# Kernel tuning notes

Measured on AMD Instinct MI355X. Metric: run time of the kernel, lower is better.

Reference implementation:

```python
import jax, jax.numpy as jnp
import numpy as np

LATENT = 256
MID = 512
T = 5          # num_transforms
OUT = T * 6 + T  # 35
THRESH = 0.9   # MATRIX_NORM_THRESHOLD
EPS = 1e-5     # torch LayerNorm eps
B = 131072


def _xavier(key, fan_in, fan_out):
    lim = np.sqrt(6.0 / (fan_in + fan_out)).astype(np.float32)
    return jax.random.uniform(key, (fan_in, fan_out), jnp.float32, -lim, lim)


def setup_inputs() -> dict:
    key = jax.random.key(0)
    ks = jax.random.split(key, 8)
    z = jax.random.normal(ks[0], (B, LATENT), jnp.float32)
    W1 = _xavier(ks[1], LATENT, MID)
    Wa = _xavier(ks[2], MID, MID)
    Wb = _xavier(ks[3], MID, MID)
    Wout = _xavier(ks[4], MID, OUT)
    bias = lambda n: jnp.full((n,), 0.01, jnp.float32)  # nn.init.constant_(bias, 0.01)
    return {
        "z": z,
        "W1": W1, "b1": bias(MID), "g1": jnp.ones((MID,), jnp.float32), "be1": jnp.zeros((MID,), jnp.float32),
        "Wa": Wa, "ba": bias(MID), "ga": jnp.ones((MID,), jnp.float32), "bea": jnp.zeros((MID,), jnp.float32),
        "Wb": Wb, "bb": bias(MID), "gb": jnp.ones((MID,), jnp.float32), "beb": jnp.zeros((MID,), jnp.float32),
        "Wout": Wout, "bout": bias(OUT),
    }


def _layernorm(x, g, b):
    mu = jnp.mean(x, axis=-1, keepdims=True)
    var = jnp.mean(jnp.square(x - mu), axis=-1, keepdims=True)
    return (x - mu) * jax.lax.rsqrt(var + EPS) * g + b


def reference(z, W1, b1, g1, be1, Wa, ba, ga, bea, Wb, bb, gb, beb, Wout, bout):
    # Linear -> LayerNorm -> ReLU
    h = jax.nn.relu(_layernorm(z @ W1 + b1, g1, be1))
    # ResidualBlock: Linear -> LN -> SiLU -> Linear -> LN, then skip add
    y = jax.nn.silu(_layernorm(h @ Wa + ba, ga, bea))
    y = _layernorm(y @ Wb + bb, gb, beb)
    h = h + y
    x = h @ Wout + bout                     # [B, 35]

    affines = x[:, : T * 6].reshape(-1, T, 2, 3)  # [B, T, 2, 3]
    logits = x[:, T * 6:]                         # [B, T]
    probs = jax.nn.softmax(logits, axis=-1)

    M = affines[..., :2]                          # [B, T, 2, 2]
    U, S, Vh = jnp.linalg.svd(M, full_matrices=False)
    Sc = jnp.minimum(S, THRESH)                   # clamp(max=0.9)
    M2 = jnp.einsum("btij,btj,btjk->btik", U, Sc, Vh)
    affines = jnp.concatenate([M2, affines[..., 2:]], axis=-1)
    return affines, probs
```

## Files before the change

### kernel.cpp

```cpp
#include <hip/hip_runtime.h>
#include <hip/hip_bf16.h>

#define BQ     131072
#define NT     5

typedef unsigned short u16;
typedef unsigned int   u32;
typedef unsigned long long u64;
typedef __attribute__((ext_vector_type(8))) short bf16x8;
typedef __attribute__((ext_vector_type(4))) float f32x4;
typedef __attribute__((ext_vector_type(2))) float f32x2;

__device__ __forceinline__ u16 f2bf(float x) {
  union { float f; u32 u; } v; v.f = x;
  u32 r = (v.u + 0x7FFFu + ((v.u >> 16) & 1u)) >> 16;
  return (u16)r;
}

__global__ __launch_bounds__(256) void transpose_cast(
    const float* __restrict__ src, u16* __restrict__ dst, int K, int N, int NP) {
  __shared__ float tile[32][33];
  int kx = blockIdx.x * 32, ny = blockIdx.y * 32;
  int tx = threadIdx.x, ty = threadIdx.y;
#pragma unroll
  for (int i = 0; i < 4; i++) {
    int k = kx + ty + i * 8, n = ny + tx;
    tile[ty + i * 8][tx] = (k < K && n < N) ? src[(size_t)k * N + n] : 0.f;
  }
  __syncthreads();
#pragma unroll
  for (int i = 0; i < 4; i++) {
    int n = ny + ty + i * 8, k = kx + tx;
    if (n < NP && k < K) dst[(size_t)n * K + k] = f2bf(tile[tx][ty + i * 8]);
  }
}

template <int K, int ACT>
__device__ __forceinline__ void layer(
    const u16* __restrict__ wt, const float* __restrict__ bias,
    const float* __restrict__ gam, const float* __restrict__ bet,
    const u16* src, u16* dst, float* sStat,
    int lane, int wid, int l15, int lg, int wfb)
{
  f32x4 acc[2][4];
#pragma unroll
  for (int m = 0; m < 2; m++)
#pragma unroll
    for (int n = 0; n < 4; n++) acc[m][n] = (f32x4){0.f, 0.f, 0.f, 0.f};

#pragma unroll
  for (int kb = 0; kb < K; kb += 32) {
    const int k0 = kb + lg * 8;
    bf16x8 a[2];
#pragma unroll
    for (int m = 0; m < 2; m++)
      a[m] = *(const bf16x8*)(wt + (size_t)(wfb + m * 16 + l15) * K + k0);
    bf16x8 bv[4];
#pragma unroll
    for (int n = 0; n < 4; n++) {
      int b = n * 16 + l15;
      int byte = (b * (K * 2) + k0 * 2) ^ ((b & 7) << 4);
      bv[n] = *(const bf16x8*)((const char*)src + byte);
    }
    __builtin_amdgcn_s_setprio(1);
#pragma unroll
    for (int m = 0; m < 2; m++)
#pragma unroll
      for (int n = 0; n < 4; n++)
        acc[m][n] = __builtin_amdgcn_mfma_f32_16x16x32_bf16(a[m], bv[n], acc[m][n], 0, 0, 0);
    __builtin_amdgcn_s_setprio(0);
  }

#pragma unroll
  for (int m = 0; m < 2; m++) {
    f32x4 bv4 = *(const f32x4*)(bias + wfb + m * 16 + lg * 4);
#pragma unroll
    for (int n = 0; n < 4; n++)
#pragma unroll
      for (int r = 0; r < 4; r++) acc[m][n][r] += bv4[r];
  }

  float s[4], q[4];
#pragma unroll
  for (int n = 0; n < 4; n++) {
    s[n] = 0.f; q[n] = 0.f;
#pragma unroll
    for (int m = 0; m < 2; m++)
#pragma unroll
      for (int r = 0; r < 4; r++) { float v = acc[m][n][r]; s[n] += v; q[n] += v * v; }
    s[n] += __shfl_xor(s[n], 16); q[n] += __shfl_xor(q[n], 16);
    s[n] += __shfl_xor(s[n], 32); q[n] += __shfl_xor(q[n], 32);
  }
  if (lg == 0) {
#pragma unroll
    for (int n = 0; n < 4; n++) {
      int b = n * 16 + l15;
      *(f32x2*)(sStat + wid * 128 + b * 2) = (f32x2){s[n], q[n]};
    }
  }
  __syncthreads();

  float ss = 0.f, qq = 0.f;
#pragma unroll
  for (int w = 0; w < 16; w++) {
    f32x2 v = *(const f32x2*)(sStat + w * 128 + lane * 2);
    ss += v[0]; qq += v[1];
  }
  float meanb = ss * (1.f / 512.f);
  float rstdb = rsqrtf(qq * (1.f / 512.f) - meanb * meanb + 1e-5f);

  float mean[4], rstd[4];
#pragma unroll
  for (int n = 0; n < 4; n++) {
    mean[n] = __shfl(meanb, n * 16 + l15);
    rstd[n] = __shfl(rstdb, n * 16 + l15);
  }

#pragma unroll
  for (int m = 0; m < 2; m++) {
    int f0 = wfb + m * 16 + lg * 4;
    f32x4 gv  = *(const f32x4*)(gam + f0);
    f32x4 bev = *(const f32x4*)(bet + f0);
#pragma unroll
    for (int n = 0; n < 4; n++) {
      int b = n * 16 + l15;
      u16 pk[4];
#pragma unroll
      for (int r = 0; r < 4; r++) {
        float v = (acc[m][n][r] - mean[n]) * rstd[n] * gv[r] + bev[r];
        if (ACT == 1) v = fmaxf(v, 0.f);
        else if (ACT == 2) v = v / (1.f + __expf(-v));
        pk[r] = f2bf(v);
      }
      u64 w64 = (u64)pk[0] | ((u64)pk[1] << 16) | ((u64)pk[2] << 32) | ((u64)pk[3] << 48);
      int byte = (b * 1024 + f0 * 2) ^ ((b & 7) << 4);
      *(u64*)((char*)dst + byte) = w64;
    }
  }
  __syncthreads();
}

__global__ __launch_bounds__(1024)
__attribute__((amdgpu_waves_per_eu(4))) void ifs_main(
    const float* __restrict__ z,
    const u16* __restrict__ wt1, const u16* __restrict__ wta,
    const u16* __restrict__ wtb, const u16* __restrict__ wtout,
    const float* __restrict__ b1, const float* __restrict__ g1, const float* __restrict__ be1,
    const float* __restrict__ ba, const float* __restrict__ ga, const float* __restrict__ bea,
    const float* __restrict__ bb, const float* __restrict__ gb, const float* __restrict__ beb,
    const float* __restrict__ bout, float* __restrict__ out)
{
  __shared__ __align__(16) char smem[65536 * 2 + 8192];
  u16*   sA    = (u16*)smem;
  u16*   sB    = (u16*)(smem + 65536);
  float* sStat = (float*)(smem + 131072);

  const int tid  = threadIdx.x;
  const int lane = tid & 63, wid = tid >> 6;
  const int l15  = lane & 15, lg = lane >> 4;
  const int bbase = blockIdx.x * 64;
  const int wfb   = wid * 32;

#pragma unroll
  for (int i = 0; i < 4; i++) {
    int c = tid + i * 1024;
    int b = c >> 6, kc = c & 63;
    const float4 v = *(const float4*)(z + (size_t)(bbase + b) * 256 + kc * 4);
    u32 lo = (u32)f2bf(v.x) | ((u32)f2bf(v.y) << 16);
    u32 hi = (u32)f2bf(v.z) | ((u32)f2bf(v.w) << 16);
    u64 pk = (u64)lo | ((u64)hi << 32);
    int byte = (b * 512 + kc * 8) ^ ((b & 7) << 4);
    *(u64*)((char*)sB + byte) = pk;
  }
  __syncthreads();

  layer<256, 1>(wt1, b1, g1, be1, sB, sA, sStat, lane, wid, l15, lg, wfb);
  layer<512, 2>(wta, ba, ga, bea, sA, sB, sStat, lane, wid, l15, lg, wfb);
  layer<512, 0>(wtb, bb, gb, beb, sB, sB, sStat, lane, wid, l15, lg, wfb);

  {
    const int nf = wid & 3, kh = wid >> 2;
    const int b  = nf * 16 + l15;
    f32x4 xacc[3];
#pragma unroll
    for (int m = 0; m < 3; m++) xacc[m] = (f32x4){0.f, 0.f, 0.f, 0.f};
#pragma unroll
    for (int kk = 0; kk < 128; kk += 32) {
      int k0 = kh * 128 + kk + lg * 8;
      int byte = (b * 1024 + k0 * 2) ^ ((b & 7) << 4);
      bf16x8 bh = *(const bf16x8*)((const char*)sA + byte);
      bf16x8 by = *(const bf16x8*)((const char*)sB + byte);
#pragma unroll
      for (int m = 0; m < 3; m++) {
        bf16x8 aw = *(const bf16x8*)(wtout + (size_t)(m * 16 + l15) * 512 + k0);
        xacc[m] = __builtin_amdgcn_mfma_f32_16x16x32_bf16(aw, bh, xacc[m], 0, 0, 0);
        xacc[m] = __builtin_amdgcn_mfma_f32_16x16x32_bf16(aw, by, xacc[m], 0, 0, 0);
      }
    }
    __syncthreads();
    float* sP = (float*)sA;
#pragma unroll
    for (int m = 0; m < 3; m++)
      *(f32x4*)(sP + (size_t)(kh * 64 + b) * 48 + m * 16 + lg * 4) = xacc[m];
    __syncthreads();
    float* sX = (float*)sB;
    if (tid < 768) {
      int b2 = tid / 12, j = (tid - b2 * 12) * 4;
      f32x4 v0 = *(const f32x4*)(sP + (size_t)(0 * 64 + b2) * 48 + j);
      f32x4 v1 = *(const f32x4*)(sP + (size_t)(1 * 64 + b2) * 48 + j);
      f32x4 v2 = *(const f32x4*)(sP + (size_t)(2 * 64 + b2) * 48 + j);
      f32x4 v3 = *(const f32x4*)(sP + (size_t)(3 * 64 + b2) * 48 + j);
#pragma unroll
      for (int r = 0; r < 4; r++) v0[r] += v1[r] + v2[r] + v3[r];
      *(f32x4*)(sX + (size_t)b2 * 48 + j) = v0;
    }
    __syncthreads();

    if (tid < 64) {
      int bb2 = tid;
      float l[5], mx = -1e30f;
#pragma unroll
      for (int j = 0; j < 5; j++) { l[j] = sX[bb2 * 48 + 30 + j] + bout[30 + j]; mx = fmaxf(mx, l[j]); }
      float ssum = 0.f, e[5];
#pragma unroll
      for (int j = 0; j < 5; j++) { e[j] = __expf(l[j] - mx); ssum += e[j]; }
      float inv = 1.f / ssum;
      float* op = out + (size_t)BQ * 30 + (size_t)(bbase + bb2) * 5;
#pragma unroll
      for (int j = 0; j < 5; j++) op[j] = e[j] * inv;
    }
    if (tid < 320) {
      int b2 = tid / 5, t = tid - b2 * 5;
      const float* xr = sX + b2 * 48 + t * 6;
      float a   = xr[0] + bout[t * 6 + 0];
      float bb_ = xr[1] + bout[t * 6 + 1];
      float tx  = xr[2] + bout[t * 6 + 2];
      float c   = xr[3] + bout[t * 6 + 3];
      float d   = xr[4] + bout[t * 6 + 4];
      float ty  = xr[5] + bout[t * 6 + 5];
      float E = 0.5f * (a + d), F = 0.5f * (a - d);
      float G = 0.5f * (c + bb_), H = 0.5f * (c - bb_);
      float Q = sqrtf(E * E + H * H), R = sqrtf(F * F + G * G);
      float sx = Q + R, sy = Q - R;
      float a1 = atan2f(G, F), a2 = atan2f(H, E);
      float th = 0.5f * (a2 - a1), ph = 0.5f * (a2 + a1);
      float sxc = fminf(sx, 0.9f);
      float syc = fminf(fmaxf(sy, -0.9f), 0.9f);
      float st, ct, sp, cp;
      __sincosf(th, &st, &ct);
      __sincosf(ph, &sp, &cp);
      float ux = cp * sxc, uy = sp * sxc, vx = sp * syc, vy = cp * syc;
      float m00 =  ux * ct - vx * st;
      float m01 = -ux * st - vx * ct;
      float m10 =  uy * ct + vy * st;
      float m11 = -uy * st + vy * ct;
      float* op = out + (size_t)(bbase + b2) * 30 + t * 6;
      op[0] = m00; op[1] = m01; op[2] = tx;
      op[3] = m10; op[4] = m11; op[5] = ty;
    }
  }
}

extern "C" void kernel_launch(void* const* d_in, const int* in_sizes, int n_in,
                              void* d_out, int out_size, void* d_ws, size_t ws_size,
                              hipStream_t stream) {
  const float* z    = (const float*)d_in[0];
  const float* W1   = (const float*)d_in[1];
  const float* b1   = (const float*)d_in[2];
  const float* g1   = (const float*)d_in[3];
  const float* be1  = (const float*)d_in[4];
  const float* Wa   = (const float*)d_in[5];
  const float* ba   = (const float*)d_in[6];
  const float* ga   = (const float*)d_in[7];
  const float* bea  = (const float*)d_in[8];
  const float* Wb   = (const float*)d_in[9];
  const float* bb   = (const float*)d_in[10];
  const float* gb   = (const float*)d_in[11];
  const float* beb  = (const float*)d_in[12];
  const float* Wout = (const float*)d_in[13];
  const float* bout = (const float*)d_in[14];
  float* out = (float*)d_out;

  char* w = (char*)d_ws;
  u16* wt1   = (u16*)(w);
  u16* wta   = (u16*)(w + 262144);
  u16* wtb   = (u16*)(w + 786432);
  u16* wtout = (u16*)(w + 1310720);

  dim3 tb(32, 8);
  transpose_cast<<<dim3(8, 16),  tb, 0, stream>>>(W1,   wt1,   256, 512, 512);
  transpose_cast<<<dim3(16, 16), tb, 0, stream>>>(Wa,   wta,   512, 512, 512);
  transpose_cast<<<dim3(16, 16), tb, 0, stream>>>(Wb,   wtb,   512, 512, 512);
  transpose_cast<<<dim3(16, 2),  tb, 0, stream>>>(Wout, wtout, 512, 35,  48);

  ifs_main<<<BQ / 64, 1024, 0, stream>>>(
      z, wt1, wta, wtb, wtout,
      b1, g1, be1, ba, ga, bea, bb, gb, beb, bout, out);
}
```

Baseline: 686.7 us.

## Stage weight K-slabs into LDS via double-buffered global_load_lds and split head pass

Each layer now streams its weights through LDS. Weights are pre-laid-out in swizzled 32-wide K slabs and copied with double-buffered global_load_lds, instead of each wave loading its weights from global memory directly. Activations are kept in a single in-place buffer. To allow this, the output head is split into two passes: one on h right after layer 1, and one on y that adds the saved partial result. The four weight prep kernels are merged into one launch. The changes add a barrier and vmcnt wait per K step, and the larger LDS footprint limits occupancy to one block per CU.

```diff
diff --git a/kernel.cpp b/kernel.cpp
--- a/kernel.cpp
+++ b/kernel.cpp
@@ -1,8 +1,8 @@
 #include <hip/hip_runtime.h>
 #include <hip/hip_bf16.h>
 
-#define BQ     131072
-#define NT     5
+#define BQ 131072
+#define NT 5
 
 typedef unsigned short u16;
 typedef unsigned int   u32;
@@ -11,64 +11,120 @@
 typedef __attribute__((ext_vector_type(4))) float f32x4;
 typedef __attribute__((ext_vector_type(2))) float f32x2;
 
+#define ACT_OFF   0
+#define WBUF_OFF  65536
+#define SX_OFF    (WBUF_OFF + 53248)
+#define XH_OFF    131072
+#define STAT_OFF  143360
+#define SMEM_SZ   151552
+
 __device__ __forceinline__ u16 f2bf(float x) {
   union { float f; u32 u; } v; v.f = x;
   u32 r = (v.u + 0x7FFFu + ((v.u >> 16) & 1u)) >> 16;
   return (u16)r;
 }
 
-__global__ __launch_bounds__(256) void transpose_cast(
-    const float* __restrict__ src, u16* __restrict__ dst, int K, int N, int NP) {
-  __shared__ float tile[32][33];
+__device__ __forceinline__ int wsw(int f, int k) {
+  return (f * 64 + k * 2) ^ ((f & 7) << 4);
+}
+
+__global__ __launch_bounds__(256) void prep_weights(
+    const float* __restrict__ s0, const float* __restrict__ s1,
+    const float* __restrict__ s2, const float* __restrict__ s3,
+    u16* __restrict__ d0, u16* __restrict__ d1,
+    u16* __restrict__ d2, u16* __restrict__ d3) {
+  const int zid = blockIdx.z;
   int kx = blockIdx.x * 32, ny = blockIdx.y * 32;
   int tx = threadIdx.x, ty = threadIdx.y;
-#pragma unroll
-  for (int i = 0; i < 4; i++) {
-    int k = kx + ty + i * 8, n = ny + tx;
-    tile[ty + i * 8][tx] = (k < K && n < N) ? src[(size_t)k * N + n] : 0.f;
-  }
-  __syncthreads();
-#pragma unroll
-  for (int i = 0; i < 4; i++) {
-    int n = ny + ty + i * 8, k = kx + tx;
-    if (n < NP && k < K) dst[(size_t)n * K + k] = f2bf(tile[tx][ty + i * 8]);
+  if (zid < 3) {
+    const float* src = (zid == 0) ? s0 : ((zid == 1) ? s1 : s2);
+    u16* dst         = (zid == 0) ? d0 : ((zid == 1) ? d1 : d2);
+    const int K = (zid == 0) ? 256 : 512;
+    if (kx >= K) return;
+#pragma unroll
+    for (int i = 0; i < 4; i++) {
+      int k = kx + ty + i * 8, n = ny + tx;
+      if (k < K) {
+        u16 v = f2bf(src[(size_t)k * 512 + n]);
+        size_t byte = (size_t)(k >> 5) * 32768 + (u32)wsw(n, k & 31);
+        *(u16*)((char*)dst + byte) = v;
+      }
+    }
+  } else {
+    if (ny >= 48) return;
+    __shared__ float tile[32][33];
+#pragma unroll
+    for (int i = 0; i < 4; i++) {
+      int k = kx + ty + i * 8, n = ny + tx;
+      tile[ty + i * 8][tx] = (k < 512 && n < 35) ? s3[(size_t)k * 35 + n] : 0.f;
+    }
+    __syncthreads();
+#pragma unroll
+    for (int i = 0; i < 4; i++) {
+      int n = ny + ty + i * 8, k = kx + tx;
+      if (n < 48) d3[(size_t)n * 512 + k] = f2bf(tile[tx][ty + i * 8]);
+    }
+  }
+}
+
+__device__ __forceinline__ void stage_slab(const u16* __restrict__ wsrc,
+                                           char* ldsdst, int wid, int lane) {
+#pragma unroll
+  for (int i = 0; i < 2; i++) {
+    int off = (wid * 2 + i) * 1024;
+    __builtin_amdgcn_global_load_lds(
+        (const __attribute__((address_space(1))) void*)((const char*)wsrc + off + lane * 16),
+        (__attribute__((address_space(3))) void*)(ldsdst + off), 16, 0, 0);
   }
 }
 
 template <int K, int ACT>
 __device__ __forceinline__ void layer(
-    const u16* __restrict__ wt, const float* __restrict__ bias,
+    const u16* __restrict__ wslabs, const float* __restrict__ bias,
     const float* __restrict__ gam, const float* __restrict__ bet,
-    const u16* src, u16* dst, float* sStat,
-    int lane, int wid, int l15, int lg, int wfb)
+    const char* src, char* dst, char* smem,
+    int tid, int lane, int wid, int l15, int lg, int wfb)
 {
+  char* wbuf   = smem + WBUF_OFF;
+  float* sStat = (float*)(smem + STAT_OFF);
+  const int SS = (K == 256) ? 512 : 1024;
+
   f32x4 acc[2][4];
 #pragma unroll
   for (int m = 0; m < 2; m++)
 #pragma unroll
     for (int n = 0; n < 4; n++) acc[m][n] = (f32x4){0.f, 0.f, 0.f, 0.f};
 
-#pragma unroll
-  for (int kb = 0; kb < K; kb += 32) {
-    const int k0 = kb + lg * 8;
-    bf16x8 a[2];
-#pragma unroll
-    for (int m = 0; m < 2; m++)
-      a[m] = *(const bf16x8*)(wt + (size_t)(wfb + m * 16 + l15) * K + k0);
+  stage_slab(wslabs, wbuf, wid, lane);
+  asm volatile("s_waitcnt vmcnt(0)" ::: "memory");
+  __syncthreads();
+
+  const int aoff0 = wsw(wfb + l15, lg * 8);
+  const int aoff1 = wsw(wfb + 16 + l15, lg * 8);
+  const int NS = K / 32;
+  for (int t = 0; t < NS; ++t) {
+    const char* slab = wbuf + (t & 1) * 32768;
+    if (t + 1 < NS)
+      stage_slab(wslabs + (size_t)(t + 1) * 16384, wbuf + ((t + 1) & 1) * 32768, wid, lane);
+    const int k0 = t * 32 + lg * 8;
+    bf16x8 a0 = *(const bf16x8*)(slab + aoff0);
+    bf16x8 a1 = *(const bf16x8*)(slab + aoff1);
     bf16x8 bv[4];
 #pragma unroll
     for (int n = 0; n < 4; n++) {
       int b = n * 16 + l15;
-      int byte = (b * (K * 2) + k0 * 2) ^ ((b & 7) << 4);
-      bv[n] = *(const bf16x8*)((const char*)src + byte);
+      int byte = (b * SS + k0 * 2) ^ ((b & 7) << 4);
+      bv[n] = *(const bf16x8*)(src + byte);
     }
     __builtin_amdgcn_s_setprio(1);
 #pragma unroll
-    for (int m = 0; m < 2; m++)
-#pragma unroll
-      for (int n = 0; n < 4; n++)
-        acc[m][n] = __builtin_amdgcn_mfma_f32_16x16x32_bf16(a[m], bv[n], acc[m][n], 0, 0, 0);
+    for (int n = 0; n < 4; n++) {
+      acc[0][n] = __builtin_amdgcn_mfma_f32_16x16x32_bf16(a0, bv[n], acc[0][n], 0, 0, 0);
+      acc[1][n] = __builtin_amdgcn_mfma_f32_16x16x32_bf16(a1, bv[n], acc[1][n], 0, 0, 0);
+    }
     __builtin_amdgcn_s_setprio(0);
+    asm volatile("s_waitcnt vmcnt(0)" ::: "memory");
+    __syncthreads();
   }
 
 #pragma unroll
@@ -134,14 +190,59 @@
       }
       u64 w64 = (u64)pk[0] | ((u64)pk[1] << 16) | ((u64)pk[2] << 32) | ((u64)pk[3] << 48);
       int byte = (b * 1024 + f0 * 2) ^ ((b & 7) << 4);
-      *(u64*)((char*)dst + byte) = w64;
-    }
-  }
-  __syncthreads();
-}
-
-__global__ __launch_bounds__(1024)
-__attribute__((amdgpu_waves_per_eu(4))) void ifs_main(
+      *(u64*)(dst + byte) = w64;
+    }
+  }
+  __syncthreads();
+}
+
+template <bool FINAL>
+__device__ __forceinline__ void head_pass(
+    const u16* __restrict__ wtout, const char* act, char* smem,
+    int tid, int wid, int l15, int lg)
+{
+  float* sP  = (float*)(smem + WBUF_OFF);
+  float* sXh = (float*)(smem + XH_OFF);
+  float* sX  = FINAL ? (float*)(smem + SX_OFF) : sXh;
+  const int nf = wid & 3, kh = wid >> 2;
+  const int b  = nf * 16 + l15;
+  f32x4 xacc[3];
+#pragma unroll
+  for (int m = 0; m < 3; m++) xacc[m] = (f32x4){0.f, 0.f, 0.f, 0.f};
+#pragma unroll
+  for (int kk = 0; kk < 128; kk += 32) {
+    int k0 = kh * 128 + kk + lg * 8;
+    int byte = (b * 1024 + k0 * 2) ^ ((b & 7) << 4);
+    bf16x8 bh = *(const bf16x8*)(act + byte);
+#pragma unroll
+    for (int m = 0; m < 3; m++) {
+      bf16x8 aw = *(const bf16x8*)(wtout + (size_t)(m * 16 + l15) * 512 + k0);
+      xacc[m] = __builtin_amdgcn_mfma_f32_16x16x32_bf16(aw, bh, xacc[m], 0, 0, 0);
+    }
+  }
+#pragma unroll
+  for (int m = 0; m < 3; m++)
+    *(f32x4*)(sP + (size_t)(kh * 64 + b) * 52 + m * 16 + lg * 4) = xacc[m];
+  __syncthreads();
+  if (tid < 768) {
+    int b2 = tid / 12, j = (tid - b2 * 12) * 4;
+    f32x4 v0 = *(const f32x4*)(sP + (size_t)(0 * 64 + b2) * 52 + j);
+    f32x4 v1 = *(const f32x4*)(sP + (size_t)(1 * 64 + b2) * 52 + j);
+    f32x4 v2 = *(const f32x4*)(sP + (size_t)(2 * 64 + b2) * 52 + j);
+    f32x4 v3 = *(const f32x4*)(sP + (size_t)(3 * 64 + b2) * 52 + j);
+#pragma unroll
+    for (int r = 0; r < 4; r++) v0[r] += v1[r] + v2[r] + v3[r];
+    if (FINAL) {
+      f32x4 vh = *(const f32x4*)(sXh + (size_t)b2 * 48 + j);
+#pragma unroll
+      for (int r = 0; r < 4; r++) v0[r] += vh[r];
+    }
+    *(f32x4*)(sX + (size_t)b2 * 48 + j) = v0;
+  }
+  __syncthreads();
+}
+
+__global__ __launch_bounds__(1024) void ifs_main(
     const float* __restrict__ z,
     const u16* __restrict__ wt1, const u16* __restrict__ wta,
     const u16* __restrict__ wtb, const u16* __restrict__ wtout,
@@ -150,16 +251,13 @@
     const float* __restrict__ bb, const float* __restrict__ gb, const float* __restrict__ beb,
     const float* __restrict__ bout, float* __restrict__ out)
 {
-  __shared__ __align__(16) char smem[65536 * 2 + 8192];
-  u16*   sA    = (u16*)smem;
-  u16*   sB    = (u16*)(smem + 65536);
-  float* sStat = (float*)(smem + 131072);
-
+  __shared__ __align__(16) char smem[SMEM_SZ];
   const int tid  = threadIdx.x;
   const int lane = tid & 63, wid = tid >> 6;
   const int l15  = lane & 15, lg = lane >> 4;
   const int bbase = blockIdx.x * 64;
   const int wfb   = wid * 32;
+  char* act = smem + ACT_OFF;
 
 #pragma unroll
   for (int i = 0; i < 4; i++) {
@@ -170,94 +268,58 @@
     u32 hi = (u32)f2bf(v.z) | ((u32)f2bf(v.w) << 16);
     u64 pk = (u64)lo | ((u64)hi << 32);
     int byte = (b * 512 + kc * 8) ^ ((b & 7) << 4);
-    *(u64*)((char*)sB + byte) = pk;
-  }
-  __syncthreads();
-
-  layer<256, 1>(wt1, b1, g1, be1, sB, sA, sStat, lane, wid, l15, lg, wfb);
-  layer<512, 2>(wta, ba, ga, bea, sA, sB, sStat, lane, wid, l15, lg, wfb);
-  layer<512, 0>(wtb, bb, gb, beb, sB, sB, sStat, lane, wid, l15, lg, wfb);
-
-  {
-    const int nf = wid & 3, kh = wid >> 2;
-    const int b  = nf * 16 + l15;
-    f32x4 xacc[3];
-#pragma unroll
-    for (int m = 0; m < 3; m++) xacc[m] = (f32x4){0.f, 0.f, 0.f, 0.f};
-#pragma unroll
-    for (int kk = 0; kk < 128; kk += 32) {
-      int k0 = kh * 128 + kk + lg * 8;
-      int byte = (b * 1024 + k0 * 2) ^ ((b & 7) << 4);
-      bf16x8 bh = *(const bf16x8*)((const char*)sA + byte);
-      bf16x8 by = *(const bf16x8*)((const char*)sB + byte);
-#pragma unroll
-      for (int m = 0; m < 3; m++) {
-        bf16x8 aw = *(const bf16x8*)(wtout + (size_t)(m * 16 + l15) * 512 + k0);
-        xacc[m] = __builtin_amdgcn_mfma_f32_16x16x32_bf16(aw, bh, xacc[m], 0, 0, 0);
-        xacc[m] = __builtin_amdgcn_mfma_f32_16x16x32_bf16(aw, by, xacc[m], 0, 0, 0);
-      }
-    }
-    __syncthreads();
-    float* sP = (float*)sA;
-#pragma unroll
-    for (int m = 0; m < 3; m++)
-      *(f32x4*)(sP + (size_t)(kh * 64 + b) * 48 + m * 16 + lg * 4) = xacc[m];
-    __syncthreads();
-    float* sX = (float*)sB;
-    if (tid < 768) {
-      int b2 = tid / 12, j = (tid - b2 * 12) * 4;
-      f32x4 v0 = *(const f32x4*)(sP + (size_t)(0 * 64 + b2) * 48 + j);
-      f32x4 v1 = *(const f32x4*)(sP + (size_t)(1 * 64 + b2) * 48 + j);
-      f32x4 v2 = *(const f32x4*)(sP + (size_t)(2 * 64 + b2) * 48 + j);
-      f32x4 v3 = *(const f32x4*)(sP + (size_t)(3 * 64 + b2) * 48 + j);
-#pragma unroll
-      for (int r = 0; r < 4; r++) v0[r] += v1[r] + v2[r] + v3[r];
-      *(f32x4*)(sX + (size_t)b2 * 48 + j) = v0;
-    }
-    __syncthreads();
-
-    if (tid < 64) {
-      int bb2 = tid;
-      float l[5], mx = -1e30f;
-#pragma unroll
-      for (int j = 0; j < 5; j++) { l[j] = sX[bb2 * 48 + 30 + j] + bout[30 + j]; mx = fmaxf(mx, l[j]); }
-      float ssum = 0.f, e[5];
-#pragma unroll
-      for (int j = 0; j < 5; j++) { e[j] = __expf(l[j] - mx); ssum += e[j]; }
-      float inv = 1.f / ssum;
-      float* op = out + (size_t)BQ * 30 + (size_t)(bbase + bb2) * 5;
-#pragma unroll
-      for (int j = 0; j < 5; j++) op[j] = e[j] * inv;
-    }
-    if (tid < 320) {
-      int b2 = tid / 5, t = tid - b2 * 5;
-      const float* xr = sX + b2 * 48 + t * 6;
-      float a   = xr[0] + bout[t * 6 + 0];
-      float bb_ = xr[1] + bout[t * 6 + 1];
-      float tx  = xr[2] + bout[t * 6 + 2];
-      float c   = xr[3] + bout[t * 6 + 3];
-      float d   = xr[4] + bout[t * 6 + 4];
-      float ty  = xr[5] + bout[t * 6 + 5];
-      float E = 0.5f * (a + d), F = 0.5f * (a - d);
-      float G = 0.5f * (c + bb_), H = 0.5f * (c - bb_);
-      float Q = sqrtf(E * E + H * H), R = sqrtf(F * F + G * G);
-      float sx = Q + R, sy = Q - R;
-      float a1 = atan2f(G, F), a2 = atan2f(H, E);
-      float th = 0.5f * (a2 - a1), ph = 0.5f * (a2 + a1);
-      float sxc = fminf(sx, 0.9f);
-      float syc = fminf(fmaxf(sy, -0.9f), 0.9f);
-      float st, ct, sp, cp;
-      __sincosf(th, &st, &ct);
-      __sincosf(ph, &sp, &cp);
-      float ux = cp * sxc, uy = sp * sxc, vx = sp * syc, vy = cp * syc;
-      float m00 =  ux * ct - vx * st;
-      float m01 = -ux * st - vx * ct;
-      float m10 =  uy * ct + vy * st;
-      float m11 = -uy * st + vy * ct;
-      float* op = out + (size_t)(bbase + b2) * 30 + t * 6;
-      op[0] = m00; op[1] = m01; op[2] = tx;
-      op[3] = m10; op[4] = m11; op[5] = ty;
-    }
+    *(u64*)(act + byte) = pk;
+  }
+  __syncthreads();
+
+  layer<256, 1>(wt1, b1, g1, be1, act, act, smem, tid, lane, wid, l15, lg, wfb);
+  head_pass<false>(wtout, act, smem, tid, wid, l15, lg);
+  layer<512, 2>(wta, ba, ga, bea, act, act, smem, tid, lane, wid, l15, lg, wfb);
+  layer<512, 0>(wtb, bb, gb, beb, act, act, smem, tid, lane, wid, l15, lg, wfb);
+  head_pass<true>(wtout, act, smem, tid, wid, l15, lg);
+
+  float* sX = (float*)(smem + SX_OFF);
+  if (tid < 64) {
+    int bb2 = tid;
+    float l[5], mx = -1e30f;
+#pragma unroll
+    for (int j = 0; j < 5; j++) { l[j] = sX[bb2 * 48 + 30 + j] + bout[30 + j]; mx = fmaxf(mx, l[j]); }
+    float ssum = 0.f, e[5];
+#pragma unroll
+    for (int j = 0; j < 5; j++) { e[j] = __expf(l[j] - mx); ssum += e[j]; }
+    float inv = 1.f / ssum;
+    float* op = out + (size_t)BQ * 30 + (size_t)(bbase + bb2) * 5;
+#pragma unroll
+    for (int j = 0; j < 5; j++) op[j] = e[j] * inv;
+  }
+  if (tid < 320) {
+    int b2 = tid / 5, t = tid - b2 * 5;
+    const float* xr = sX + b2 * 48 + t * 6;
+    float a   = xr[0] + bout[t * 6 + 0];
+    float bb_ = xr[1] + bout[t * 6 + 1];
+    float tx  = xr[2] + bout[t * 6 + 2];
+    float c   = xr[3] + bout[t * 6 + 3];
+    float d   = xr[4] + bout[t * 6 + 4];
+    float ty  = xr[5] + bout[t * 6 + 5];
+    float E = 0.5f * (a + d), F = 0.5f * (a - d);
+    float G = 0.5f * (c + bb_), H = 0.5f * (c - bb_);
+    float Q = sqrtf(E * E + H * H), R = sqrtf(F * F + G * G);
+    float sx = Q + R, sy = Q - R;
+    float a1 = atan2f(G, F), a2 = atan2f(H, E);
+    float th = 0.5f * (a2 - a1), ph = 0.5f * (a2 + a1);
+    float sxc = fminf(sx, 0.9f);
+    float syc = fminf(fmaxf(sy, -0.9f), 0.9f);
+    float st, ct, sp, cp;
+    __sincosf(th, &st, &ct);
+    __sincosf(ph, &sp, &cp);
+    float ux = cp * sxc, uy = sp * sxc, vx = sp * syc, vy = cp * syc;
+    float m00 =  ux * ct - vx * st;
+    float m01 = -ux * st - vx * ct;
+    float m10 =  uy * ct + vy * st;
+    float m11 = -uy * st + vy * ct;
+    float* op = out + (size_t)(bbase + b2) * 30 + t * 6;
+    op[0] = m00; op[1] = m01; op[2] = tx;
+    op[3] = m10; op[4] = m11; op[5] = ty;
   }
 }
 
@@ -287,11 +349,8 @@
   u16* wtb   = (u16*)(w + 786432);
   u16* wtout = (u16*)(w + 1310720);
 
-  dim3 tb(32, 8);
-  transpose_cast<<<dim3(8, 16),  tb, 0, stream>>>(W1,   wt1,   256, 512, 512);
-  transpose_cast<<<dim3(16, 16), tb, 0, stream>>>(Wa,   wta,   512, 512, 512);
-  transpose_cast<<<dim3(16, 16), tb, 0, stream>>>(Wb,   wtb,   512, 512, 512);
-  transpose_cast<<<dim3(16, 2),  tb, 0, stream>>>(Wout, wtout, 512, 35,  48);
+  prep_weights<<<dim3(16, 16, 4), dim3(32, 8), 0, stream>>>(
+      W1, Wa, Wb, Wout, wt1, wta, wtb, wtout);
 
   ifs_main<<<BQ / 64, 1024, 0, stream>>>(
       z, wt1, wta, wtb, wtout,
```

Measured after the change: 735.0 us. 7.0% more time.
